# Kernel tuning notes

Measured on AMD Instinct MI355X. Metric: run time of the kernel, lower is better.

The kernel has to match this reference:

```python
import jax, jax.numpy as jnp
import numpy as np

N = 100000      # nodes (== hyperedges, H is square: adjacency-derived incidence)
NNZ = 3200000   # nonzeros in H
IN, HID, OUT = 512, 16, 64


def setup_inputs() -> dict:
    key = jax.random.key(0)
    ks = jax.random.split(key, 8)
    row = jax.random.randint(ks[0], (NNZ,), 0, N)
    col = jax.random.randint(ks[1], (NNZ,), 0, N)
    values = jnp.ones((NNZ,), dtype=jnp.float32)
    X = jax.random.normal(ks[2], (N, IN), dtype=jnp.float32)
    W1 = jax.random.normal(ks[3], (HID, IN), dtype=jnp.float32) * 0.05
    b1 = jax.random.normal(ks[4], (HID,), dtype=jnp.float32) * 0.05
    W2 = jax.random.normal(ks[5], (OUT, HID), dtype=jnp.float32) * 0.05
    b2 = jax.random.normal(ks[6], (OUT,), dtype=jnp.float32) * 0.05
    return {"row": row, "col": col, "values": values, "X": X,
            "W1": W1, "b1": b1, "W2": W2, "b2": b2}


def reference(row, col, values, X, W1, b1, W2, b2):
    # Degrees: d_V = H.sum(1) over rows, d_E = H.sum(0) over cols
    d_V = jax.ops.segment_sum(values, row, num_segments=N)
    d_E = jax.ops.segment_sum(values, col, num_segments=N)
    dv = d_V ** -0.5          # D_V^-1/2 diagonal
    de = d_E ** -1.0          # D_E^-1 diagonal (W = I, folded in)

    def conv(Y):
        # D_V^-1/2 @ H @ D_E^-1 @ H^T @ D_V^-1/2 @ Y, via edge-list SpMMs
        Y1 = Y * dv[:, None]
        # Z = H^T @ Y1 : scatter v * Y1[row] into hyperedge bins (col)
        Z = jax.ops.segment_sum(values[:, None] * Y1[row], col, num_segments=N)
        Z = Z * de[:, None]
        # O = H @ Z : scatter v * Z[col] back into node bins (row)
        O = jax.ops.segment_sum(values[:, None] * Z[col], row, num_segments=N)
        return O * dv[:, None]

    # dropout is identity in eval mode
    H1 = jax.nn.relu(conv(X @ W1.T + b1))      # [N, HID]
    out = conv(H1 @ W2.T + b2)                  # [N, OUT]
    return out
```

## Files before the change

kernel.cpp:

```cpp
#include <hip/hip_runtime.h>

#define NN 100000
#define NNZ 3200000
#define DIN 512
#define DHID 16
#define DOUT 64
#define NBUK 391
#define BCAP 9216
#define EPB 4096
#define NBLK_A ((NNZ + EPB - 1) / EPB)

#define GLOBAL_AS __attribute__((address_space(1)))
#define LDS_AS    __attribute__((address_space(3)))


__global__ __launch_bounds__(256) void init_cur_kernel(
    int* __restrict__ cur_c, int* __restrict__ cur_r) {
    int i = blockIdx.x * 256 + threadIdx.x;
    if (i < NBUK) { cur_c[i] = i * BCAP; cur_r[i] = i * BCAP; }
}

__global__ __launch_bounds__(256) void bucket_scatter_kernel(
    const int* __restrict__ row, const int* __restrict__ col,
    int* __restrict__ cur_c, int* __restrict__ cur_r,
    int* __restrict__ stgc, int* __restrict__ stgr) {
    __shared__ int stage[EPB];
    __shared__ unsigned short binOf[EPB];
    __shared__ int histc[512], histr[512], scn[256], lof[512], curb[512], gdelta[512];
    int tid = threadIdx.x;
    int m = NNZ - blockIdx.x * EPB; if (m > EPB) m = EPB;
    int e0 = blockIdx.x * EPB + tid;

    histc[tid] = 0; histc[tid + 256] = 0;
    histr[tid] = 0; histr[tid + 256] = 0;
    __syncthreads();
    #pragma unroll 4
    for (int u = 0; u < EPB / 256; ++u) {
        if (tid + u * 256 < m) {
            int e = e0 + u * 256;
            atomicAdd(&histc[col[e] >> 8], 1);
            atomicAdd(&histr[row[e] >> 8], 1);
        }
    }
    __syncthreads();

    for (int side = 0; side < 2; ++side) {
        const int* key = side ? row : col;
        const int* oth = side ? col : row;
        int* gcur = side ? cur_r : cur_c;
        int* gstg = side ? stgr : stgc;
        const int* hist = side ? histr : histc;

        int s0 = hist[2 * tid], s1 = hist[2 * tid + 1];
        int ps = s0 + s1;
        scn[tid] = ps;
        __syncthreads();
        for (int d = 1; d < 256; d <<= 1) {
            int t = (tid >= d) ? scn[tid - d] : 0;
            __syncthreads();
            scn[tid] += t;
            __syncthreads();
        }
        int excl = scn[tid] - ps;
        lof[2 * tid] = excl;
        lof[2 * tid + 1] = excl + s0;
        curb[2 * tid] = excl;
        curb[2 * tid + 1] = excl + s0;
        if (2 * tid < NBUK)
            gdelta[2 * tid] = (s0 ? atomicAdd(&gcur[2 * tid], s0) : (2 * tid) * BCAP) - excl;
        if (2 * tid + 1 < NBUK)
            gdelta[2 * tid + 1] = (s1 ? atomicAdd(&gcur[2 * tid + 1], s1) : (2 * tid + 1) * BCAP) - (excl + s0);
        __syncthreads();
        #pragma unroll 2
        for (int u = 0; u < EPB / 256; ++u) {
            if (tid + u * 256 < m) {
                int e = e0 + u * 256;
                int k = key[e], o2 = oth[e];
                int bin = k >> 8;
                int pos = atomicAdd(&curb[bin], 1);
                stage[pos] = ((k & 255) << 17) | o2;
                binOf[pos] = (unsigned short)bin;
            }
        }
        __syncthreads();
        for (int i = tid; i < m; i += 256) {
            int bin = binOf[i];
            int dst = gdelta[bin] + i;
            if (dst < (bin + 1) * BCAP) gstg[dst] = stage[i];
        }
        __syncthreads();
    }
}

__global__ __launch_bounds__(256) void bucket_finalize_kernel(
    const int* __restrict__ cur_c, const int* __restrict__ cur_r,
    const int* __restrict__ stgc, const int* __restrict__ stgr,
    int* __restrict__ adjc, int* __restrict__ adjr,
    int* __restrict__ os_c, int* __restrict__ oe_c,
    int* __restrict__ os_r, int* __restrict__ oe_r,
    float* __restrict__ dee, float* __restrict__ dvv) {
    int side = blockIdx.y;
    const int* curv = side ? cur_r : cur_c;
    const int* stg = side ? stgr : stgc;
    int* adj = side ? adjr : adjc;
    int* os = side ? os_r : os_c;
    int* oe = side ? oe_r : oe_c;
    __shared__ int E[BCAP];
    __shared__ int hist[256], cur[256], scn[256];
    int b = blockIdx.x, tid = threadIdx.x;
    int base = b * BCAP;
    int m = curv[b] - base;
    if (m > BCAP) m = BCAP;
    hist[tid] = 0;
    __syncthreads();
    for (int i = tid; i < m; i += 256) {
        int ev = stg[base + i];
        E[i] = ev;
        atomicAdd(&hist[ev >> 17], 1);
    }
    __syncthreads();
    int x = hist[tid];
    scn[tid] = x;
    __syncthreads();
    for (int d = 1; d < 256; d <<= 1) {
        int t = (tid >= d) ? scn[tid - d] : 0;
        __syncthreads();
        scn[tid] += t;
        __syncthreads();
    }
    int excl = scn[tid] - x;
    cur[tid] = excl;
    __syncthreads();
    for (int i = tid; i < m; i += 256) {
        int ev = E[i];
        int nl = ev >> 17;
        int pos = atomicAdd(&cur[nl], 1);
        adj[base + pos] = ev & 0x1FFFF;
    }
    int n = (b << 8) + tid;
    if (n < NN) {
        os[n] = base + excl;
        oe[n] = base + excl + x;
        float xf = (float)x;
        if (side == 0) dee[n] = x > 0 ? 1.0f / xf : 0.f;
        else           dvv[n] = x > 0 ? rsqrtf(xf) : 0.f;
    }
}

__global__ __launch_bounds__(256) void gemm1_kernel(
    const float* __restrict__ X, const float* __restrict__ W1,
    const float* __restrict__ b1, const float* __restrict__ dvv,
    float* __restrict__ Yv) {
    __shared__ float W1s[16 * 516];
    __shared__ float Xs[16 * 260];
    int tid = threadIdx.x;
    for (int it = 0; it < 8; ++it) {
        int idx = (it * 256 + tid) << 2;
        int h = idx >> 9, k = idx & 511;
        __builtin_amdgcn_global_load_lds(
            (const GLOBAL_AS void*)(W1 + idx),
            (LDS_AS void*)(W1s + h * 516 + k), 16, 0, 0);
    }
    int n0 = blockIdx.x << 4;
    int n = tid >> 4, h = tid & 15;
    float4 a4 = make_float4(0.f, 0.f, 0.f, 0.f);
    for (int ck = 0; ck < 512; ck += 256) {
        __syncthreads();
        for (int it = 0; it < 4; ++it) {
            int idx = (it * 256 + tid) << 2;
            int r = idx >> 8, k = idx & 255;
            __builtin_amdgcn_global_load_lds(
                (const GLOBAL_AS void*)(X + (size_t)(n0 + r) * DIN + ck + k),
                (LDS_AS void*)(Xs + r * 260 + k), 16, 0, 0);
        }
        __syncthreads();
        const float4* xr = reinterpret_cast<const float4*>(Xs + n * 260);
        const float4* wr = reinterpret_cast<const float4*>(W1s + h * 516 + ck);
        #pragma unroll 8
        for (int k4 = 0; k4 < 64; ++k4) {
            float4 xv = xr[k4], wv = wr[k4];
            a4.x = fmaf(xv.x, wv.x, a4.x);
            a4.y = fmaf(xv.y, wv.y, a4.y);
            a4.z = fmaf(xv.z, wv.z, a4.z);
            a4.w = fmaf(xv.w, wv.w, a4.w);
        }
    }
    float acc = (a4.x + a4.y) + (a4.z + a4.w);
    int node = n0 + n;
    Yv[node * DHID + h] = (acc + b1[h]) * dvv[node];
}

template<int MODE, int FUSE1>
__global__ __launch_bounds__(256) void gather16_kernel(
    const int* __restrict__ os, const int* __restrict__ oe,
    const int* __restrict__ adj, const float* __restrict__ src,
    const float* __restrict__ sc, const float* __restrict__ src1,
    const float* __restrict__ sc1, float* __restrict__ dst,
    float* __restrict__ dst1) {
    int t = blockIdx.x * 256 + threadIdx.x;
    if (t >= NN * 16) return;
    int n = t >> 4, sub = (t >> 3) & 1, f2 = t & 7;
    const float2* src2 = reinterpret_cast<const float2*>(src);
    float2 a0 = make_float2(0.f, 0.f);
    float2 a1 = make_float2(0.f, 0.f);
    float2 a2 = make_float2(0.f, 0.f);
    float2 a3 = make_float2(0.f, 0.f);
    float acc1 = 0.f;
    int pe = oe[n];
    int p = os[n] + sub;
    for (; p + 6 < pe; p += 8) {
        int j0 = adj[p], j1 = adj[p + 2], j2 = adj[p + 4], j3 = adj[p + 6];
        float2 s0 = src2[(j0 << 3) | f2];
        float2 s1 = src2[(j1 << 3) | f2];
        float2 s2 = src2[(j2 << 3) | f2];
        float2 s3 = src2[(j3 << 3) | f2];
        a0.x += s0.x; a0.y += s0.y;
        a1.x += s1.x; a1.y += s1.y;
        a2.x += s2.x; a2.y += s2.y;
        a3.x += s3.x; a3.y += s3.y;
        if (FUSE1 && f2 == 0) acc1 += (src1[j0] + src1[j1]) + (src1[j2] + src1[j3]);
    }
    for (; p < pe; p += 2) {
        int j0 = adj[p];
        float2 s0 = src2[(j0 << 3) | f2];
        a0.x += s0.x; a0.y += s0.y;
        if (FUSE1 && f2 == 0) acc1 += src1[j0];
    }
    float2 acc = make_float2((a0.x + a1.x) + (a2.x + a3.x),
                             (a0.y + a1.y) + (a2.y + a3.y));
    acc.x += __shfl_xor(acc.x, 8);
    acc.y += __shfl_xor(acc.y, 8);
    if (FUSE1 && f2 == 0) acc1 += __shfl_xor(acc1, 8);
    if (sub == 0) {
        float s = sc[n];
        if (MODE == 1) {
            acc.x *= s; acc.y *= s;
        } else {
            acc.x = s * fmaxf(s * acc.x, 0.f);
            acc.y = s * fmaxf(s * acc.y, 0.f);
        }
        reinterpret_cast<float2*>(dst)[(n << 3) | f2] = acc;
        if (FUSE1 && f2 == 0) dst1[n] = acc1 * sc1[n];
    }
}

__global__ __launch_bounds__(256) void gemm2f_kernel(
    const float* __restrict__ T, const float* __restrict__ g,
    const float* __restrict__ W2, const float* __restrict__ b2,
    float* __restrict__ out) {
    int t = blockIdx.x * 256 + threadIdx.x;
    if (t >= NN * DOUT) return;
    int n = t >> 6, o = t & 63;
    const float* trow = T + n * DHID;
    const float* wrow = W2 + o * DHID;
    float acc = 0.f;
    #pragma unroll
    for (int h = 0; h < DHID; ++h) acc = fmaf(trow[h], wrow[h], acc);
    out[t] = acc + g[n] * b2[o];
}

extern "C" void kernel_launch(void* const* d_in, const int* in_sizes, int n_in,
                              void* d_out, int out_size, void* d_ws, size_t ws_size,
                              hipStream_t stream) {
    const int*   row    = (const int*)d_in[0];
    const int*   col    = (const int*)d_in[1];
    const float* X      = (const float*)d_in[3];
    const float* W1     = (const float*)d_in[4];
    const float* b1     = (const float*)d_in[5];
    const float* W2     = (const float*)d_in[6];
    const float* b2     = (const float*)d_in[7];
    float* out = (float*)d_out;

    char* ws = (char*)d_ws;
    size_t o = 0;
    auto alloc = [&](size_t elems) {
        void* p = ws + o; o += (elems * 4 + 15) & ~size_t(15); return p;
    };

    int*   cur_c = (int*)alloc(NBUK);
    int*   cur_r = (int*)alloc(NBUK);
    int*   os_c  = (int*)alloc(NN);
    int*   oe_c  = (int*)alloc(NN);
    int*   os_r  = (int*)alloc(NN);
    int*   oe_r  = (int*)alloc(NN);
    float* dvv   = (float*)alloc(NN);
    float* dee   = (float*)alloc(NN);
    float* ue    = (float*)alloc(NN);
    float* gv    = (float*)alloc(NN);
    int*   stgc  = (int*)alloc((size_t)NBUK * BCAP);
    int*   stgr  = (int*)alloc((size_t)NBUK * BCAP);
    int*   adjc  = (int*)alloc((size_t)NBUK * BCAP);
    int*   adjr  = (int*)alloc((size_t)NBUK * BCAP);
    float* Yv    = (float*)alloc((size_t)NN * DHID);
    float* Z1    = (float*)alloc((size_t)NN * DHID);
    float* Sv    = (float*)alloc((size_t)NN * DHID);
    float* Z2    = (float*)alloc((size_t)NN * DHID);
    float* Tv    = (float*)alloc((size_t)NN * DHID);

    init_cur_kernel<<<dim3((NBUK + 255) / 256), dim3(256), 0, stream>>>(cur_c, cur_r);
    bucket_scatter_kernel<<<dim3(NBLK_A), dim3(256), 0, stream>>>(
        row, col, cur_c, cur_r, stgc, stgr);
    bucket_finalize_kernel<<<dim3(NBUK, 2), dim3(256), 0, stream>>>(
        cur_c, cur_r, stgc, stgr, adjc, adjr, os_c, oe_c, os_r, oe_r, dee, dvv);

    gemm1_kernel<<<dim3(NN / 16), dim3(256), 0, stream>>>(X, W1, b1, dvv, Yv);

    int gblk = (NN * 16 + 255) / 256;
    gather16_kernel<1, 1><<<dim3(gblk), dim3(256), 0, stream>>>(
        os_c, oe_c, adjc, Yv, dee, dvv, dee, Z1, ue);
    gather16_kernel<2, 1><<<dim3(gblk), dim3(256), 0, stream>>>(
        os_r, oe_r, adjr, Z1, dvv, ue, dvv, Sv, gv);

    gather16_kernel<1, 0><<<dim3(gblk), dim3(256), 0, stream>>>(
        os_c, oe_c, adjc, Sv, dee, nullptr, nullptr, Z2, nullptr);
    gather16_kernel<1, 0><<<dim3(gblk), dim3(256), 0, stream>>>(
        os_r, oe_r, adjr, Z2, dvv, nullptr, nullptr, Tv, nullptr);

    gemm2f_kernel<<<dim3((NN * DOUT + 255) / 256), dim3(256), 0, stream>>>(
        Tv, gv, W2, b2, out);
}
```

Baseline: 411.5 us.

## Fuse final GEMM into last gather and split bucket scatter by side

The final W2 projection and bias term move into the epilogue of the last row-side gather. Each 16-lane group shuffles the scaled hidden vector and computes 64 outputs from W2 staged in LDS. This removes the Tv intermediate and the separate gemm2f launch. Separately, the bucket scatter kernel now uses a second grid dimension for the col/row side, so each block handles one side only. That doubles the block count and halves per-block serial work, at the cost of re-reading the shared index arrays.

```diff
diff --git a/kernel.cpp b/kernel.cpp
--- a/kernel.cpp
+++ b/kernel.cpp
@@ -26,69 +26,59 @@
     int* __restrict__ stgc, int* __restrict__ stgr) {
     __shared__ int stage[EPB];
     __shared__ unsigned short binOf[EPB];
-    __shared__ int histc[512], histr[512], scn[256], lof[512], curb[512], gdelta[512];
+    __shared__ int hist[512], scn[256], lof[512], curb[512], gdelta[512];
+    int side = blockIdx.y;
+    const int* key = side ? row : col;
+    const int* oth = side ? col : row;
+    int* gcur = side ? cur_r : cur_c;
+    int* gstg = side ? stgr : stgc;
     int tid = threadIdx.x;
     int m = NNZ - blockIdx.x * EPB; if (m > EPB) m = EPB;
     int e0 = blockIdx.x * EPB + tid;
 
-    histc[tid] = 0; histc[tid + 256] = 0;
-    histr[tid] = 0; histr[tid + 256] = 0;
+    hist[tid] = 0; hist[tid + 256] = 0;
     __syncthreads();
     #pragma unroll 4
+    for (int u = 0; u < EPB / 256; ++u) {
+        if (tid + u * 256 < m) atomicAdd(&hist[key[e0 + u * 256] >> 8], 1);
+    }
+    __syncthreads();
+    int s0 = hist[2 * tid], s1 = hist[2 * tid + 1];
+    int ps = s0 + s1;
+    scn[tid] = ps;
+    __syncthreads();
+    for (int d = 1; d < 256; d <<= 1) {
+        int t = (tid >= d) ? scn[tid - d] : 0;
+        __syncthreads();
+        scn[tid] += t;
+        __syncthreads();
+    }
+    int excl = scn[tid] - ps;
+    lof[2 * tid] = excl;
+    lof[2 * tid + 1] = excl + s0;
+    curb[2 * tid] = excl;
+    curb[2 * tid + 1] = excl + s0;
+    if (2 * tid < NBUK)
+        gdelta[2 * tid] = (s0 ? atomicAdd(&gcur[2 * tid], s0) : (2 * tid) * BCAP) - excl;
+    if (2 * tid + 1 < NBUK)
+        gdelta[2 * tid + 1] = (s1 ? atomicAdd(&gcur[2 * tid + 1], s1) : (2 * tid + 1) * BCAP) - (excl + s0);
+    __syncthreads();
+    #pragma unroll 2
     for (int u = 0; u < EPB / 256; ++u) {
         if (tid + u * 256 < m) {
             int e = e0 + u * 256;
-            atomicAdd(&histc[col[e] >> 8], 1);
-            atomicAdd(&histr[row[e] >> 8], 1);
-        }
-    }
-    __syncthreads();
-
-    for (int side = 0; side < 2; ++side) {
-        const int* key = side ? row : col;
-        const int* oth = side ? col : row;
-        int* gcur = side ? cur_r : cur_c;
-        int* gstg = side ? stgr : stgc;
-        const int* hist = side ? histr : histc;
-
-        int s0 = hist[2 * tid], s1 = hist[2 * tid + 1];
-        int ps = s0 + s1;
-        scn[tid] = ps;
-        __syncthreads();
-        for (int d = 1; d < 256; d <<= 1) {
-            int t = (tid >= d) ? scn[tid - d] : 0;
-            __syncthreads();
-            scn[tid] += t;
-            __syncthreads();
-        }
-        int excl = scn[tid] - ps;
-        lof[2 * tid] = excl;
-        lof[2 * tid + 1] = excl + s0;
-        curb[2 * tid] = excl;
-        curb[2 * tid + 1] = excl + s0;
-        if (2 * tid < NBUK)
-            gdelta[2 * tid] = (s0 ? atomicAdd(&gcur[2 * tid], s0) : (2 * tid) * BCAP) - excl;
-        if (2 * tid + 1 < NBUK)
-            gdelta[2 * tid + 1] = (s1 ? atomicAdd(&gcur[2 * tid + 1], s1) : (2 * tid + 1) * BCAP) - (excl + s0);
-        __syncthreads();
-        #pragma unroll 2
-        for (int u = 0; u < EPB / 256; ++u) {
-            if (tid + u * 256 < m) {
-                int e = e0 + u * 256;
-                int k = key[e], o2 = oth[e];
-                int bin = k >> 8;
-                int pos = atomicAdd(&curb[bin], 1);
-                stage[pos] = ((k & 255) << 17) | o2;
-                binOf[pos] = (unsigned short)bin;
-            }
-        }
-        __syncthreads();
-        for (int i = tid; i < m; i += 256) {
-            int bin = binOf[i];
-            int dst = gdelta[bin] + i;
-            if (dst < (bin + 1) * BCAP) gstg[dst] = stage[i];
-        }
-        __syncthreads();
+            int k = key[e], o2 = oth[e];
+            int bin = k >> 8;
+            int pos = atomicAdd(&curb[bin], 1);
+            stage[pos] = ((k & 255) << 17) | o2;
+            binOf[pos] = (unsigned short)bin;
+        }
+    }
+    __syncthreads();
+    for (int i = tid; i < m; i += 256) {
+        int bin = binOf[i];
+        int dst = gdelta[bin] + i;
+        if (dst < (bin + 1) * BCAP) gstg[dst] = stage[i];
     }
 }
 
@@ -190,15 +180,29 @@
     Yv[node * DHID + h] = (acc + b1[h]) * dvv[node];
 }
 
-template<int MODE, int FUSE1>
+template<int MODE, int FUSE1, int FUSEOUT>
 __global__ __launch_bounds__(256) void gather16_kernel(
     const int* __restrict__ os, const int* __restrict__ oe,
     const int* __restrict__ adj, const float* __restrict__ src,
     const float* __restrict__ sc, const float* __restrict__ src1,
     const float* __restrict__ sc1, float* __restrict__ dst,
-    float* __restrict__ dst1) {
-    int t = blockIdx.x * 256 + threadIdx.x;
-    if (t >= NN * 16) return;
+    float* __restrict__ dst1, const float* __restrict__ W2,
+    const float* __restrict__ b2, const float* __restrict__ g1,
+    float* __restrict__ outp) {
+    __shared__ float W2t[16 * 64];
+    __shared__ float b2s[64];
+    int tid = threadIdx.x;
+    if (FUSEOUT) {
+        #pragma unroll
+        for (int q = 0; q < 4; ++q) {
+            int idx = (tid << 2) + q;
+            int o = idx >> 4, h = idx & 15;
+            W2t[h * 64 + o] = W2[idx];
+        }
+        if (tid < 64) b2s[tid] = b2[tid];
+        __syncthreads();
+    }
+    int t = blockIdx.x * 256 + tid;
     int n = t >> 4, sub = (t >> 3) & 1, f2 = t & 7;
     const float2* src2 = reinterpret_cast<const float2*>(src);
     float2 a0 = make_float2(0.f, 0.f);
@@ -231,7 +235,32 @@
     acc.x += __shfl_xor(acc.x, 8);
     acc.y += __shfl_xor(acc.y, 8);
     if (FUSE1 && f2 == 0) acc1 += __shfl_xor(acc1, 8);
-    if (sub == 0) {
+    if (FUSEOUT) {
+        float s = sc[n];
+        float T[16];
+        #pragma unroll
+        for (int q = 0; q < 8; ++q) {
+            T[2 * q]     = s * __shfl(acc.x, q, 16);
+            T[2 * q + 1] = s * __shfl(acc.y, q, 16);
+        }
+        int l = tid & 15;
+        float gn = g1[n];
+        float4 o4 = make_float4(0.f, 0.f, 0.f, 0.f);
+        #pragma unroll
+        for (int h = 0; h < DHID; ++h) {
+            float4 w = *reinterpret_cast<const float4*>(&W2t[h * 64 + 4 * l]);
+            o4.x = fmaf(T[h], w.x, o4.x);
+            o4.y = fmaf(T[h], w.y, o4.y);
+            o4.z = fmaf(T[h], w.z, o4.z);
+            o4.w = fmaf(T[h], w.w, o4.w);
+        }
+        float4 bb = *reinterpret_cast<const float4*>(&b2s[4 * l]);
+        o4.x = fmaf(gn, bb.x, o4.x);
+        o4.y = fmaf(gn, bb.y, o4.y);
+        o4.z = fmaf(gn, bb.z, o4.z);
+        o4.w = fmaf(gn, bb.w, o4.w);
+        reinterpret_cast<float4*>(outp)[(n << 4) | l] = o4;
+    } else if (sub == 0) {
         float s = sc[n];
         if (MODE == 1) {
             acc.x *= s; acc.y *= s;
@@ -242,21 +271,6 @@
         reinterpret_cast<float2*>(dst)[(n << 3) | f2] = acc;
         if (FUSE1 && f2 == 0) dst1[n] = acc1 * sc1[n];
     }
-}
-
-__global__ __launch_bounds__(256) void gemm2f_kernel(
-    const float* __restrict__ T, const float* __restrict__ g,
-    const float* __restrict__ W2, const float* __restrict__ b2,
-    float* __restrict__ out) {
-    int t = blockIdx.x * 256 + threadIdx.x;
-    if (t >= NN * DOUT) return;
-    int n = t >> 6, o = t & 63;
-    const float* trow = T + n * DHID;
-    const float* wrow = W2 + o * DHID;
-    float acc = 0.f;
-    #pragma unroll
-    for (int h = 0; h < DHID; ++h) acc = fmaf(trow[h], wrow[h], acc);
-    out[t] = acc + g[n] * b2[o];
 }
 
 extern "C" void kernel_launch(void* const* d_in, const int* in_sizes, int n_in,
@@ -295,27 +309,27 @@
     float* Z1    = (float*)alloc((size_t)NN * DHID);
     float* Sv    = (float*)alloc((size_t)NN * DHID);
     float* Z2    = (float*)alloc((size_t)NN * DHID);
-    float* Tv    = (float*)alloc((size_t)NN * DHID);
 
     init_cur_kernel<<<dim3((NBUK + 255) / 256), dim3(256), 0, stream>>>(cur_c, cur_r);
-    bucket_scatter_kernel<<<dim3(NBLK_A), dim3(256), 0, stream>>>(
+    bucket_scatter_kernel<<<dim3(NBLK_A, 2), dim3(256), 0, stream>>>(
         row, col, cur_c, cur_r, stgc, stgr);
     bucket_finalize_kernel<<<dim3(NBUK, 2), dim3(256), 0, stream>>>(
         cur_c, cur_r, stgc, stgr, adjc, adjr, os_c, oe_c, os_r, oe_r, dee, dvv);
 
     gemm1_kernel<<<dim3(NN / 16), dim3(256), 0, stream>>>(X, W1, b1, dvv, Yv);
 
-    int gblk = (NN * 16 + 255) / 256;
-    gather16_kernel<1, 1><<<dim3(gblk), dim3(256), 0, stream>>>(
-        os_c, oe_c, adjc, Yv, dee, dvv, dee, Z1, ue);
-    gather16_kernel<2, 1><<<dim3(gblk), dim3(256), 0, stream>>>(
-        os_r, oe_r, adjr, Z1, dvv, ue, dvv, Sv, gv);
-
-    gather16_kernel<1, 0><<<dim3(gblk), dim3(256), 0, stream>>>(
-        os_c, oe_c, adjc, Sv, dee, nullptr, nullptr, Z2, nullptr);
-    gather16_kernel<1, 0><<<dim3(gblk), dim3(256), 0, stream>>>(
-        os_r, oe_r, adjr, Z2, dvv, nullptr, nullptr, Tv, nullptr);
-
-    gemm2f_kernel<<<dim3((NN * DOUT + 255) / 256), dim3(256), 0, stream>>>(
-        Tv, gv, W2, b2, out);
-}
+    int gblk = NN * 16 / 256;
+    gather16_kernel<1, 1, 0><<<dim3(gblk), dim3(256), 0, stream>>>(
+        os_c, oe_c, adjc, Yv, dee, dvv, dee, Z1, ue,
+        nullptr, nullptr, nullptr, nullptr);
+    gather16_kernel<2, 1, 0><<<dim3(gblk), dim3(256), 0, stream>>>(
+        os_r, oe_r, adjr, Z1, dvv, ue, dvv, Sv, gv,
+        nullptr, nullptr, nullptr, nullptr);
+
+    gather16_kernel<1, 0, 0><<<dim3(gblk), dim3(256), 0, stream>>>(
+        os_c, oe_c, adjc, Sv, dee, nullptr, nullptr, Z2, nullptr,
+        nullptr, nullptr, nullptr, nullptr);
+    gather16_kernel<1, 0, 1><<<dim3(gblk), dim3(256), 0, stream>>>(
+        os_r, oe_r, adjr, Z2, dvv, nullptr, nullptr, nullptr, nullptr,
+        W2, b2, gv, out);
+}
```

After: 361.1 us. 12.2% less time.
